# Optimization experiments

Hardware: AMD Instinct MI355X
Metric: run time of the kernel (lower is better)

## Reference

```python
import jax, jax.numpy as jnp
import numpy as np

N_NODES = 100000

def gcn_conv(x, edge_index, W, b):
    # normalize=False GCNConv: out[i] = sum_{(j->i) in E} (x W)[j] + b
    h = x @ W                                   # [N, out_dim]
    src, dst = edge_index[0], edge_index[1]
    msgs = h[src]                               # [E, out_dim]
    agg = jax.ops.segment_sum(msgs, dst, num_segments=N_NODES)
    return agg + b

def setup_inputs() -> dict:
    key = jax.random.key(0)
    k1, k2, k3, k4 = jax.random.split(key, 4)
    x = jax.random.normal(k1, (N_NODES, 512), dtype=jnp.float32)
    edge_index = jax.random.randint(k2, (2, 3200000), 0, N_NODES, dtype=jnp.int64)
    W1 = jax.random.normal(k3, (512, 16), dtype=jnp.float32) * (1.0 / np.sqrt(512))
    b1 = jnp.zeros((16,), dtype=jnp.float32)
    W2 = jax.random.normal(k4, (16, 40), dtype=jnp.float32) * (1.0 / np.sqrt(16))
    b2 = jnp.zeros((40,), dtype=jnp.float32)
    return {"x": x, "edge_index": edge_index, "W1": W1, "b1": b1, "W2": W2, "b2": b2}

def reference(x, edge_index, W1, b1, W2, b2):
    h = jax.nn.relu(gcn_conv(x, edge_index, W1, b1))
    # dropout is identity at inference (training=False)
    out = gcn_conv(h, edge_index, W2, b2)
    return jax.nn.log_softmax(out, axis=1)
```

## Files before the change

kernel.cpp:

```cpp
#include <hip/hip_runtime.h>
#include <math.h>

#define N_NODES 100000
#define N_EDGES 3200000
#define BSHIFT 7
#define BNODES 128
#define NB 782
#define PLACE_BLOCKS 400
#define G1_S 68

typedef float vfloat4 __attribute__((ext_vector_type(4)));

__global__ __launch_bounds__(64) void gemm1_kernel(
    const float* __restrict__ x, const float* __restrict__ W1,
    float* __restrict__ h, int nrows)
{
    __shared__ __align__(16) float xs[32 * G1_S];
    const int t = threadIdx.x;
    const int rbase = blockIdx.x * 64;

    const int kl4  = (t & 7) * 4;
    const int rstg = t >> 3;
    const int swz  = (t & 7) << 3;

    const int rq = t >> 2;
    const int cg = t & 3;
    const float4* __restrict__ w4 = (const float4*)W1;

    float4 acc0 = make_float4(0.f, 0.f, 0.f, 0.f);
    float4 acc1 = acc0, acc2 = acc0, acc3 = acc0;

    vfloat4 pre[8];
    #pragma unroll
    for (int i = 0; i < 8; ++i) {
        int rg = rbase + rstg + i * 8;
        pre[i] = (rg < nrows)
            ? __builtin_nontemporal_load(
                  (const vfloat4*)(x + (size_t)rg * 512 + kl4))
            : (vfloat4){0.f, 0.f, 0.f, 0.f};
    }

    for (int kc = 0; kc < 512; kc += 32) {
        #pragma unroll
        for (int i = 0; i < 8; ++i) {
            int row = (rstg + i * 8) ^ swz;
            float* p = xs + kl4 * G1_S + row;
            p[0 * G1_S] = pre[i].x;
            p[1 * G1_S] = pre[i].y;
            p[2 * G1_S] = pre[i].z;
            p[3 * G1_S] = pre[i].w;
        }
        if (kc + 32 < 512) {
            #pragma unroll
            for (int i = 0; i < 8; ++i) {
                int rg = rbase + rstg + i * 8;
                pre[i] = (rg < nrows)
                    ? __builtin_nontemporal_load(
                          (const vfloat4*)(x + (size_t)rg * 512 + kc + 32 + kl4))
                    : (vfloat4){0.f, 0.f, 0.f, 0.f};
            }
        }

        #pragma unroll
        for (int k4 = 0; k4 < 8; ++k4) {
            const int k0 = k4 * 4;
            const int rr = (rq * 4) ^ (k4 << 3);
            float4 xv0 = *(const float4*)(xs + (k0 + 0) * G1_S + rr);
            float4 xv1 = *(const float4*)(xs + (k0 + 1) * G1_S + rr);
            float4 xv2 = *(const float4*)(xs + (k0 + 2) * G1_S + rr);
            float4 xv3 = *(const float4*)(xs + (k0 + 3) * G1_S + rr);
            float4 wv0 = w4[(kc + k0 + 0) * 4 + cg];
            float4 wv1 = w4[(kc + k0 + 1) * 4 + cg];
            float4 wv2 = w4[(kc + k0 + 2) * 4 + cg];
            float4 wv3 = w4[(kc + k0 + 3) * 4 + cg];

            #define GCN_UPD(xv, wv)                                           \
                acc0.x += (xv).x * (wv).x; acc0.y += (xv).x * (wv).y;         \
                acc0.z += (xv).x * (wv).z; acc0.w += (xv).x * (wv).w;         \
                acc1.x += (xv).y * (wv).x; acc1.y += (xv).y * (wv).y;         \
                acc1.z += (xv).y * (wv).z; acc1.w += (xv).y * (wv).w;         \
                acc2.x += (xv).z * (wv).x; acc2.y += (xv).z * (wv).y;         \
                acc2.z += (xv).z * (wv).z; acc2.w += (xv).z * (wv).w;         \
                acc3.x += (xv).w * (wv).x; acc3.y += (xv).w * (wv).y;         \
                acc3.z += (xv).w * (wv).z; acc3.w += (xv).w * (wv).w;
            GCN_UPD(xv0, wv0)
            GCN_UPD(xv1, wv1)
            GCN_UPD(xv2, wv2)
            GCN_UPD(xv3, wv3)
            #undef GCN_UPD
        }
    }

    {
        int rg = rbase + rq * 4;
        if (rg + 0 < nrows) *(float4*)(h + (size_t)(rg + 0) * 16 + cg * 4) = acc0;
        if (rg + 1 < nrows) *(float4*)(h + (size_t)(rg + 1) * 16 + cg * 4) = acc1;
        if (rg + 2 < nrows) *(float4*)(h + (size_t)(rg + 2) * 16 + cg * 4) = acc2;
        if (rg + 3 < nrows) *(float4*)(h + (size_t)(rg + 3) * 16 + cg * 4) = acc3;
    }
}

__global__ __launch_bounds__(256) void bin_count_kernel(
    const int* __restrict__ ei, int* __restrict__ bucket_cnt)
{
    __shared__ int hist[NB];
    const int t = threadIdx.x;
    for (int i = t; i < NB; i += 256) hist[i] = 0;
    __syncthreads();
    const int stride = gridDim.x * 256;
    for (int e = blockIdx.x * 256 + t; e < N_EDGES; e += stride)
        atomicAdd(&hist[ei[N_EDGES + e] >> BSHIFT], 1);
    __syncthreads();
    for (int i = t; i < NB; i += 256)
        if (hist[i]) atomicAdd(&bucket_cnt[i], hist[i]);
}

__global__ __launch_bounds__(1024) void bucket_scan_kernel(
    const int* __restrict__ bucket_cnt, int* __restrict__ bucket_base,
    int* __restrict__ bucket_cursor)
{
    __shared__ int s[1024];
    const int t = threadIdx.x;
    s[t] = (t < NB) ? bucket_cnt[t] : 0;
    __syncthreads();
    for (int off = 1; off < 1024; off <<= 1) {
        int v = (t >= off) ? s[t - off] : 0;
        __syncthreads();
        s[t] += v;
        __syncthreads();
    }
    if (t < NB) {
        int excl = (t == 0) ? 0 : s[t - 1];
        bucket_base[t]   = excl;
        bucket_cursor[t] = excl;
        if (t == NB - 1) bucket_base[NB] = s[t];
    }
}

__global__ __launch_bounds__(256) void bin_place_kernel(
    const int* __restrict__ ei, int* __restrict__ bucket_cursor,
    int* __restrict__ packed)
{
    __shared__ int cnt[NB];
    __shared__ int base_off[NB];
    __shared__ int cur[NB];
    const int t = threadIdx.x;
    const int chunk = (N_EDGES + PLACE_BLOCKS - 1) / PLACE_BLOCKS;
    const int cs = blockIdx.x * chunk;
    const int ce = min(cs + chunk, N_EDGES);

    for (int i = t; i < NB; i += 256) { cnt[i] = 0; cur[i] = 0; }
    __syncthreads();
    for (int e = cs + t; e < ce; e += 256)
        atomicAdd(&cnt[ei[N_EDGES + e] >> BSHIFT], 1);
    __syncthreads();
    for (int i = t; i < NB; i += 256)
        base_off[i] = cnt[i] ? atomicAdd(&bucket_cursor[i], cnt[i]) : 0;
    __syncthreads();
    for (int e = cs + t; e < ce; e += 256) {
        int s = ei[e];
        int d = ei[N_EDGES + e];
        int b = d >> BSHIFT;
        int pos = base_off[b] + atomicAdd(&cur[b], 1);
        packed[pos] = s | ((d & (BNODES - 1)) << 17);
    }
}

__global__ __launch_bounds__(256) void csr_sort_kernel(
    const int* __restrict__ bucket_base, const int* __restrict__ packed,
    int* __restrict__ csr_src, int* __restrict__ row_ptr)
{
    __shared__ int hist[BNODES];
    __shared__ int excl[BNODES];
    __shared__ int cur[BNODES];
    __shared__ int scan[BNODES];
    const int t = threadIdx.x;
    const int b = blockIdx.x;
    if (t < BNODES) { hist[t] = 0; cur[t] = 0; }
    __syncthreads();

    const int bs = bucket_base[b];
    const int be = bucket_base[b + 1];
    for (int e = bs + t; e < be; e += 256)
        atomicAdd(&hist[packed[e] >> 17], 1);
    __syncthreads();

    if (t < BNODES) scan[t] = hist[t];
    __syncthreads();
    for (int off = 1; off < BNODES; off <<= 1) {
        int v = (t < BNODES && t >= off) ? scan[t - off] : 0;
        __syncthreads();
        if (t < BNODES) scan[t] += v;
        __syncthreads();
    }
    if (t < BNODES) {
        int ex = (t == 0) ? 0 : scan[t - 1];
        excl[t] = ex;
        int g = b * BNODES + t;
        if (g < N_NODES) row_ptr[g] = bs + ex;
    }
    if (b == NB - 1 && t == 0) row_ptr[N_NODES] = N_EDGES;
    __syncthreads();

    for (int e = bs + t; e < be; e += 256) {
        int p  = packed[e];
        int dl = p >> 17;
        int pos = bs + excl[dl] + atomicAdd(&cur[dl], 1);
        csr_src[pos] = p & 0x1FFFF;
    }
}

__global__ __launch_bounds__(256) void gather1_kernel(
    const int* __restrict__ row_ptr, const int* __restrict__ csr_src,
    const float* __restrict__ h, const float* __restrict__ b1,
    float* __restrict__ h1)
{
    const int node = (blockIdx.x * 256 + threadIdx.x) >> 6;
    if (node >= N_NODES) return;
    const int lane = threadIdx.x & 63;
    const int c = lane & 15, slot = lane >> 4;
    const int start = row_ptr[node], end = row_ptr[node + 1];

    float acc = 0.f;
    int e = start;
    for (; e + 16 <= end; e += 16) {
        int s0 = csr_src[e + slot * 4 + 0];
        int s1 = csr_src[e + slot * 4 + 1];
        int s2 = csr_src[e + slot * 4 + 2];
        int s3 = csr_src[e + slot * 4 + 3];
        float v0 = h[s0 * 16 + c];
        float v1 = h[s1 * 16 + c];
        float v2 = h[s2 * 16 + c];
        float v3 = h[s3 * 16 + c];
        acc += (v0 + v1) + (v2 + v3);
    }
    for (; e + 4 <= end; e += 4)
        acc += h[csr_src[e + slot] * 16 + c];
    if (e + slot < end)
        acc += h[csr_src[e + slot] * 16 + c];

    acc += __shfl_xor(acc, 16);
    acc += __shfl_xor(acc, 32);
    if (lane < 16)
        h1[(size_t)node * 16 + c] = fmaxf(acc + b1[c], 0.f);
}

__global__ __launch_bounds__(256) void gather2_kernel(
    const int* __restrict__ row_ptr, const int* __restrict__ csr_src,
    const float* __restrict__ h1, const float* __restrict__ W2,
    const float* __restrict__ b2, float* __restrict__ out)
{
    const int node = (blockIdx.x * 256 + threadIdx.x) >> 6;
    if (node >= N_NODES) return;
    const int lane = threadIdx.x & 63;
    const int c = lane & 15, slot = lane >> 4;

    float w2c[16];
    float b2v = 0.f;
    if (lane < 40) {
        b2v = b2[lane];
        #pragma unroll
        for (int k = 0; k < 16; ++k) w2c[k] = W2[k * 40 + lane];
    } else {
        #pragma unroll
        for (int k = 0; k < 16; ++k) w2c[k] = 0.f;
    }

    const int start = row_ptr[node], end = row_ptr[node + 1];
    float acc = 0.f;
    int e = start;
    for (; e + 16 <= end; e += 16) {
        int s0 = csr_src[e + slot * 4 + 0];
        int s1 = csr_src[e + slot * 4 + 1];
        int s2 = csr_src[e + slot * 4 + 2];
        int s3 = csr_src[e + slot * 4 + 3];
        float v0 = h1[s0 * 16 + c];
        float v1 = h1[s1 * 16 + c];
        float v2 = h1[s2 * 16 + c];
        float v3 = h1[s3 * 16 + c];
        acc += (v0 + v1) + (v2 + v3);
    }
    for (; e + 4 <= end; e += 4)
        acc += h1[csr_src[e + slot] * 16 + c];
    if (e + slot < end)
        acc += h1[csr_src[e + slot] * 16 + c];

    acc += __shfl_xor(acc, 16);
    acc += __shfl_xor(acc, 32);

    float z = b2v;
    #pragma unroll
    for (int k = 0; k < 16; ++k)
        z += __shfl(acc, k) * w2c[k];

    float zm = (lane < 40) ? z : -1e30f;
    #pragma unroll
    for (int off = 1; off < 64; off <<= 1)
        zm = fmaxf(zm, __shfl_xor(zm, off));
    float ex = (lane < 40) ? __expf(z - zm) : 0.f;
    float sum = ex;
    #pragma unroll
    for (int off = 1; off < 64; off <<= 1)
        sum += __shfl_xor(sum, off);
    const float lse = zm + __logf(sum);

    if (lane < 40)
        out[(size_t)node * 40 + lane] = z - lse;
}

extern "C" void kernel_launch(void* const* d_in, const int* in_sizes, int n_in,
                              void* d_out, int out_size, void* d_ws, size_t ws_size,
                              hipStream_t stream)
{
    const float* x  = (const float*)d_in[0];
    const int*   ei = (const int*)d_in[1];
    const float* W1 = (const float*)d_in[2];
    const float* b1 = (const float*)d_in[3];
    const float* W2 = (const float*)d_in[4];
    const float* b2 = (const float*)d_in[5];
    float* out = (float*)d_out;

    float* h      = (float*)d_ws;
    int*   csr    = (int*)(h + (size_t)N_NODES * 16);
    int*   packed = csr + N_EDGES;
    float* h1     = (float*)packed;
    int*   rowp   = packed + N_EDGES;
    int*   bcnt   = rowp + (N_NODES + 1);
    int*   bbase  = bcnt + NB;
    int*   bcur   = bbase + (NB + 1);

    const int gemm1_blocks  = (N_NODES + 63) / 64;
    const int gather_blocks = (N_NODES + 3) / 4;

    hipMemsetAsync(bcnt, 0, NB * sizeof(int), stream);
    bin_count_kernel  <<<256, 256, 0, stream>>>(ei, bcnt);
    bucket_scan_kernel<<<1, 1024, 0, stream>>>(bcnt, bbase, bcur);
    bin_place_kernel  <<<PLACE_BLOCKS, 256, 0, stream>>>(ei, bcur, packed);
    csr_sort_kernel   <<<NB, 256, 0, stream>>>(bbase, packed, csr, rowp);

    gemm1_kernel<<<gemm1_blocks, 64, 0, stream>>>(x, W1, h, N_NODES);

    gather1_kernel<<<gather_blocks, 256, 0, stream>>>(rowp, csr, h, b1, h1);
    gather2_kernel<<<gather_blocks, 256, 0, stream>>>(rowp, csr, h1, W2, b2, out);
}
```

Before: 545.3 us.

## Split first GEMM into tiles co-scheduled with CSR-build kernels

```diff
diff --git a/kernel.cpp b/kernel.cpp
--- a/kernel.cpp
+++ b/kernel.cpp
@@ -8,23 +8,27 @@
 #define NB 782
 #define PLACE_BLOCKS 400
 #define G1_S 68
+#define G1_TILES 1563
+#define TILES_A 280
+#define TILES_B 600
+#define TILES_C (G1_TILES - TILES_A - TILES_B)
+#define BINCNT_BLOCKS 256
 
 typedef float vfloat4 __attribute__((ext_vector_type(4)));
 
-__global__ __launch_bounds__(64) void gemm1_kernel(
+__device__ __forceinline__ void gemm1_tile(
+    int tile, int lane,
     const float* __restrict__ x, const float* __restrict__ W1,
-    float* __restrict__ h, int nrows)
-{
-    __shared__ __align__(16) float xs[32 * G1_S];
-    const int t = threadIdx.x;
-    const int rbase = blockIdx.x * 64;
-
-    const int kl4  = (t & 7) * 4;
-    const int rstg = t >> 3;
-    const int swz  = (t & 7) << 3;
-
-    const int rq = t >> 2;
-    const int cg = t & 3;
+    float* __restrict__ h, float* __restrict__ xs )
+{
+    if (tile >= G1_TILES) return;
+    const int rbase = tile * 64;
+
+    const int kl4  = (lane & 7) * 4;
+    const int rstg = lane >> 3;
+    const int swz  = (lane & 7) << 3;
+    const int rq   = lane >> 2;
+    const int cg   = lane & 3;
     const float4* __restrict__ w4 = (const float4*)W1;
 
     float4 acc0 = make_float4(0.f, 0.f, 0.f, 0.f);
@@ -34,7 +38,7 @@
     #pragma unroll
     for (int i = 0; i < 8; ++i) {
         int rg = rbase + rstg + i * 8;
-        pre[i] = (rg < nrows)
+        pre[i] = (rg < N_NODES)
             ? __builtin_nontemporal_load(
                   (const vfloat4*)(x + (size_t)rg * 512 + kl4))
             : (vfloat4){0.f, 0.f, 0.f, 0.f};
@@ -54,7 +58,7 @@
             #pragma unroll
             for (int i = 0; i < 8; ++i) {
                 int rg = rbase + rstg + i * 8;
-                pre[i] = (rg < nrows)
+                pre[i] = (rg < N_NODES)
                     ? __builtin_nontemporal_load(
                           (const vfloat4*)(x + (size_t)rg * 512 + kc + 32 + kl4))
                     : (vfloat4){0.f, 0.f, 0.f, 0.f};
@@ -93,26 +97,41 @@
 
     {
         int rg = rbase + rq * 4;
-        if (rg + 0 < nrows) *(float4*)(h + (size_t)(rg + 0) * 16 + cg * 4) = acc0;
-        if (rg + 1 < nrows) *(float4*)(h + (size_t)(rg + 1) * 16 + cg * 4) = acc1;
-        if (rg + 2 < nrows) *(float4*)(h + (size_t)(rg + 2) * 16 + cg * 4) = acc2;
-        if (rg + 3 < nrows) *(float4*)(h + (size_t)(rg + 3) * 16 + cg * 4) = acc3;
-    }
-}
-
-__global__ __launch_bounds__(256) void bin_count_kernel(
+        if (rg + 0 < N_NODES) *(float4*)(h + (size_t)(rg + 0) * 16 + cg * 4) = acc0;
+        if (rg + 1 < N_NODES) *(float4*)(h + (size_t)(rg + 1) * 16 + cg * 4) = acc1;
+        if (rg + 2 < N_NODES) *(float4*)(h + (size_t)(rg + 2) * 16 + cg * 4) = acc2;
+        if (rg + 3 < N_NODES) *(float4*)(h + (size_t)(rg + 3) * 16 + cg * 4) = acc3;
+    }
+}
+
+union ShA {
+    float xs[4][32 * G1_S];
+    int hist[NB];
+};
+
+__global__ __launch_bounds__(256) void stageA_kernel(
+    const float* __restrict__ x, const float* __restrict__ W1,
+    float* __restrict__ h,
     const int* __restrict__ ei, int* __restrict__ bucket_cnt)
 {
-    __shared__ int hist[NB];
+    __shared__ __align__(16) ShA sh;
     const int t = threadIdx.x;
-    for (int i = t; i < NB; i += 256) hist[i] = 0;
-    __syncthreads();
-    const int stride = gridDim.x * 256;
-    for (int e = blockIdx.x * 256 + t; e < N_EDGES; e += stride)
-        atomicAdd(&hist[ei[N_EDGES + e] >> BSHIFT], 1);
-    __syncthreads();
-    for (int i = t; i < NB; i += 256)
-        if (hist[i]) atomicAdd(&bucket_cnt[i], hist[i]);
+
+    if (blockIdx.x < BINCNT_BLOCKS) {
+        for (int i = t; i < NB; i += 256) sh.hist[i] = 0;
+        __syncthreads();
+        const int stride = BINCNT_BLOCKS * 256;
+        for (int e = blockIdx.x * 256 + t; e < N_EDGES; e += stride)
+            atomicAdd(&sh.hist[ei[N_EDGES + e] >> BSHIFT], 1);
+        __syncthreads();
+        for (int i = t; i < NB; i += 256)
+            if (sh.hist[i]) atomicAdd(&bucket_cnt[i], sh.hist[i]);
+    } else {
+        const int w = t >> 6;
+        const int tile = (blockIdx.x - BINCNT_BLOCKS) * 4 + w;
+        if (tile < TILES_A)
+            gemm1_tile(tile, t & 63, x, W1, h, sh.xs[w]);
+    }
 }
 
 __global__ __launch_bounds__(1024) void bucket_scan_kernel(
@@ -137,76 +156,101 @@
     }
 }
 
-__global__ __launch_bounds__(256) void bin_place_kernel(
+union ShB {
+    float xs[4][32 * G1_S];
+    struct { int cnt[NB]; int base_off[NB]; int cur[NB]; } p;
+};
+
+__global__ __launch_bounds__(256) void stageB_kernel(
+    const float* __restrict__ x, const float* __restrict__ W1,
+    float* __restrict__ h,
     const int* __restrict__ ei, int* __restrict__ bucket_cursor,
     int* __restrict__ packed)
 {
-    __shared__ int cnt[NB];
-    __shared__ int base_off[NB];
-    __shared__ int cur[NB];
+    __shared__ __align__(16) ShB sh;
     const int t = threadIdx.x;
-    const int chunk = (N_EDGES + PLACE_BLOCKS - 1) / PLACE_BLOCKS;
-    const int cs = blockIdx.x * chunk;
-    const int ce = min(cs + chunk, N_EDGES);
-
-    for (int i = t; i < NB; i += 256) { cnt[i] = 0; cur[i] = 0; }
-    __syncthreads();
-    for (int e = cs + t; e < ce; e += 256)
-        atomicAdd(&cnt[ei[N_EDGES + e] >> BSHIFT], 1);
-    __syncthreads();
-    for (int i = t; i < NB; i += 256)
-        base_off[i] = cnt[i] ? atomicAdd(&bucket_cursor[i], cnt[i]) : 0;
-    __syncthreads();
-    for (int e = cs + t; e < ce; e += 256) {
-        int s = ei[e];
-        int d = ei[N_EDGES + e];
-        int b = d >> BSHIFT;
-        int pos = base_off[b] + atomicAdd(&cur[b], 1);
-        packed[pos] = s | ((d & (BNODES - 1)) << 17);
-    }
-}
-
-__global__ __launch_bounds__(256) void csr_sort_kernel(
+
+    if (blockIdx.x < PLACE_BLOCKS) {
+        const int chunk = (N_EDGES + PLACE_BLOCKS - 1) / PLACE_BLOCKS;
+        const int cs = blockIdx.x * chunk;
+        const int ce = min(cs + chunk, N_EDGES);
+
+        for (int i = t; i < NB; i += 256) { sh.p.cnt[i] = 0; sh.p.cur[i] = 0; }
+        __syncthreads();
+        for (int e = cs + t; e < ce; e += 256)
+            atomicAdd(&sh.p.cnt[ei[N_EDGES + e] >> BSHIFT], 1);
+        __syncthreads();
+        for (int i = t; i < NB; i += 256)
+            sh.p.base_off[i] = sh.p.cnt[i] ? atomicAdd(&bucket_cursor[i], sh.p.cnt[i]) : 0;
+        __syncthreads();
+        for (int e = cs + t; e < ce; e += 256) {
+            int s = ei[e];
+            int d = ei[N_EDGES + e];
+            int b = d >> BSHIFT;
+            int pos = sh.p.base_off[b] + atomicAdd(&sh.p.cur[b], 1);
+            packed[pos] = s | ((d & (BNODES - 1)) << 17);
+        }
+    } else {
+        const int w = t >> 6;
+        const int tile = TILES_A + (blockIdx.x - PLACE_BLOCKS) * 4 + w;
+        if (tile < TILES_A + TILES_B)
+            gemm1_tile(tile, t & 63, x, W1, h, sh.xs[w]);
+    }
+}
+
+union ShC {
+    float xs[4][32 * G1_S];
+    struct { int hist[BNODES]; int excl[BNODES]; int cur[BNODES]; int scan[BNODES]; } c;
+};
+
+__global__ __launch_bounds__(256) void stageC_kernel(
+    const float* __restrict__ x, const float* __restrict__ W1,
+    float* __restrict__ h,
     const int* __restrict__ bucket_base, const int* __restrict__ packed,
     int* __restrict__ csr_src, int* __restrict__ row_ptr)
 {
-    __shared__ int hist[BNODES];
-    __shared__ int excl[BNODES];
-    __shared__ int cur[BNODES];
-    __shared__ int scan[BNODES];
+    __shared__ __align__(16) ShC sh;
     const int t = threadIdx.x;
     const int b = blockIdx.x;
-    if (t < BNODES) { hist[t] = 0; cur[t] = 0; }
-    __syncthreads();
-
-    const int bs = bucket_base[b];
-    const int be = bucket_base[b + 1];
-    for (int e = bs + t; e < be; e += 256)
-        atomicAdd(&hist[packed[e] >> 17], 1);
-    __syncthreads();
-
-    if (t < BNODES) scan[t] = hist[t];
-    __syncthreads();
-    for (int off = 1; off < BNODES; off <<= 1) {
-        int v = (t < BNODES && t >= off) ? scan[t - off] : 0;
-        __syncthreads();
-        if (t < BNODES) scan[t] += v;
-        __syncthreads();
-    }
-    if (t < BNODES) {
-        int ex = (t == 0) ? 0 : scan[t - 1];
-        excl[t] = ex;
-        int g = b * BNODES + t;
-        if (g < N_NODES) row_ptr[g] = bs + ex;
-    }
-    if (b == NB - 1 && t == 0) row_ptr[N_NODES] = N_EDGES;
-    __syncthreads();
-
-    for (int e = bs + t; e < be; e += 256) {
-        int p  = packed[e];
-        int dl = p >> 17;
-        int pos = bs + excl[dl] + atomicAdd(&cur[dl], 1);
-        csr_src[pos] = p & 0x1FFFF;
+
+    if (b < NB) {
+        if (t < BNODES) { sh.c.hist[t] = 0; sh.c.cur[t] = 0; }
+        __syncthreads();
+
+        const int bs = bucket_base[b];
+        const int be = bucket_base[b + 1];
+        for (int e = bs + t; e < be; e += 256)
+            atomicAdd(&sh.c.hist[packed[e] >> 17], 1);
+        __syncthreads();
+
+        if (t < BNODES) sh.c.scan[t] = sh.c.hist[t];
+        __syncthreads();
+        for (int off = 1; off < BNODES; off <<= 1) {
+            int v = (t < BNODES && t >= off) ? sh.c.scan[t - off] : 0;
+            __syncthreads();
+            if (t < BNODES) sh.c.scan[t] += v;
+            __syncthreads();
+        }
+        if (t < BNODES) {
+            int ex = (t == 0) ? 0 : sh.c.scan[t - 1];
+            sh.c.excl[t] = ex;
+            int g = b * BNODES + t;
+            if (g < N_NODES) row_ptr[g] = bs + ex;
+        }
+        if (b == NB - 1 && t == 0) row_ptr[N_NODES] = N_EDGES;
+        __syncthreads();
+
+        for (int e = bs + t; e < be; e += 256) {
+            int p  = packed[e];
+            int dl = p >> 17;
+            int pos = bs + sh.c.excl[dl] + atomicAdd(&sh.c.cur[dl], 1);
+            csr_src[pos] = p & 0x1FFFF;
+        }
+    } else {
+        const int w = t >> 6;
+        const int tile = TILES_A + TILES_B + (b - NB) * 4 + w;
+        if (tile < G1_TILES)
+            gemm1_tile(tile, t & 63, x, W1, h, sh.xs[w]);
     }
 }
 
@@ -329,16 +373,16 @@
     int*   bbase  = bcnt + NB;
     int*   bcur   = bbase + (NB + 1);
 
-    const int gemm1_blocks  = (N_NODES + 63) / 64;
+    const int stageA_blocks = BINCNT_BLOCKS + (TILES_A + 3) / 4;
+    const int stageB_blocks = PLACE_BLOCKS + (TILES_B + 3) / 4;
+    const int stageC_blocks = NB + (TILES_C + 3) / 4;
     const int gather_blocks = (N_NODES + 3) / 4;
 
     hipMemsetAsync(bcnt, 0, NB * sizeof(int), stream);
-    bin_count_kernel  <<<256, 256, 0, stream>>>(ei, bcnt);
+    stageA_kernel     <<<stageA_blocks, 256, 0, stream>>>(x, W1, h, ei, bcnt);
     bucket_scan_kernel<<<1, 1024, 0, stream>>>(bcnt, bbase, bcur);
-    bin_place_kernel  <<<PLACE_BLOCKS, 256, 0, stream>>>(ei, bcur, packed);
-    csr_sort_kernel   <<<NB, 256, 0, stream>>>(bbase, packed, csr, rowp);
-
-    gemm1_kernel<<<gemm1_blocks, 64, 0, stream>>>(x, W1, h, N_NODES);
+    stageB_kernel     <<<stageB_blocks, 256, 0, stream>>>(x, W1, h, ei, bcur, packed);
+    stageC_kernel     <<<stageC_blocks, 256, 0, stream>>>(x, W1, h, bbase, packed, csr, rowp);
 
     gather1_kernel<<<gather_blocks, 256, 0, stream>>>(rowp, csr, h, b1, h1);
     gather2_kernel<<<gather_blocks, 256, 0, stream>>>(rowp, csr, h1, W2, b2, out);
```

After: 595.7 us. +9.2%, slower.

## Drop per-node CSR sort; aggregate bucketed edges via LDS atomics per block

Applied to the files above, without the earlier changes.

```diff
diff --git a/kernel.cpp b/kernel.cpp
--- a/kernel.cpp
+++ b/kernel.cpp
@@ -8,6 +8,7 @@
 #define NB 782
 #define PLACE_BLOCKS 400
 #define G1_S 68
+#define AGG_S 17
 
 typedef float vfloat4 __attribute__((ext_vector_type(4)));
 
@@ -22,9 +23,8 @@
     const int kl4  = (t & 7) * 4;
     const int rstg = t >> 3;
     const int swz  = (t & 7) << 3;
-
-    const int rq = t >> 2;
-    const int cg = t & 3;
+    const int rq   = t >> 2;
+    const int cg   = t & 3;
     const float4* __restrict__ w4 = (const float4*)W1;
 
     float4 acc0 = make_float4(0.f, 0.f, 0.f, 0.f);
@@ -166,94 +166,69 @@
     }
 }
 
-__global__ __launch_bounds__(256) void csr_sort_kernel(
+__global__ __launch_bounds__(256) void gatherA_kernel(
     const int* __restrict__ bucket_base, const int* __restrict__ packed,
-    int* __restrict__ csr_src, int* __restrict__ row_ptr)
-{
-    __shared__ int hist[BNODES];
-    __shared__ int excl[BNODES];
-    __shared__ int cur[BNODES];
-    __shared__ int scan[BNODES];
-    const int t = threadIdx.x;
-    const int b = blockIdx.x;
-    if (t < BNODES) { hist[t] = 0; cur[t] = 0; }
-    __syncthreads();
-
-    const int bs = bucket_base[b];
-    const int be = bucket_base[b + 1];
-    for (int e = bs + t; e < be; e += 256)
-        atomicAdd(&hist[packed[e] >> 17], 1);
-    __syncthreads();
-
-    if (t < BNODES) scan[t] = hist[t];
-    __syncthreads();
-    for (int off = 1; off < BNODES; off <<= 1) {
-        int v = (t < BNODES && t >= off) ? scan[t - off] : 0;
-        __syncthreads();
-        if (t < BNODES) scan[t] += v;
-        __syncthreads();
-    }
-    if (t < BNODES) {
-        int ex = (t == 0) ? 0 : scan[t - 1];
-        excl[t] = ex;
-        int g = b * BNODES + t;
-        if (g < N_NODES) row_ptr[g] = bs + ex;
-    }
-    if (b == NB - 1 && t == 0) row_ptr[N_NODES] = N_EDGES;
-    __syncthreads();
-
-    for (int e = bs + t; e < be; e += 256) {
-        int p  = packed[e];
-        int dl = p >> 17;
-        int pos = bs + excl[dl] + atomicAdd(&cur[dl], 1);
-        csr_src[pos] = p & 0x1FFFF;
-    }
-}
-
-__global__ __launch_bounds__(256) void gather1_kernel(
-    const int* __restrict__ row_ptr, const int* __restrict__ csr_src,
     const float* __restrict__ h, const float* __restrict__ b1,
     float* __restrict__ h1)
 {
-    const int node = (blockIdx.x * 256 + threadIdx.x) >> 6;
-    if (node >= N_NODES) return;
-    const int lane = threadIdx.x & 63;
-    const int c = lane & 15, slot = lane >> 4;
-    const int start = row_ptr[node], end = row_ptr[node + 1];
-
-    float acc = 0.f;
-    int e = start;
-    for (; e + 16 <= end; e += 16) {
-        int s0 = csr_src[e + slot * 4 + 0];
-        int s1 = csr_src[e + slot * 4 + 1];
-        int s2 = csr_src[e + slot * 4 + 2];
-        int s3 = csr_src[e + slot * 4 + 3];
-        float v0 = h[s0 * 16 + c];
-        float v1 = h[s1 * 16 + c];
-        float v2 = h[s2 * 16 + c];
-        float v3 = h[s3 * 16 + c];
-        acc += (v0 + v1) + (v2 + v3);
-    }
-    for (; e + 4 <= end; e += 4)
-        acc += h[csr_src[e + slot] * 16 + c];
-    if (e + slot < end)
-        acc += h[csr_src[e + slot] * 16 + c];
-
-    acc += __shfl_xor(acc, 16);
-    acc += __shfl_xor(acc, 32);
-    if (lane < 16)
-        h1[(size_t)node * 16 + c] = fmaxf(acc + b1[c], 0.f);
-}
-
-__global__ __launch_bounds__(256) void gather2_kernel(
-    const int* __restrict__ row_ptr, const int* __restrict__ csr_src,
+    __shared__ float agg[BNODES * AGG_S];
+    const int t = threadIdx.x;
+    const int b = blockIdx.x;
+    const int c = t & 15, slot = t >> 4;
+
+    #pragma unroll
+    for (int i = 0; i < 9; ++i) {
+        int idx = i * 256 + t;
+        if (idx < BNODES * AGG_S) agg[idx] = 0.f;
+    }
+    __syncthreads();
+
+    const int bs = bucket_base[b];
+    const int nE = bucket_base[b + 1] - bs;
+
+    int i = slot;
+    for (; i + 48 < nE; i += 64) {
+        int p0 = packed[bs + i];
+        int p1 = packed[bs + i + 16];
+        int p2 = packed[bs + i + 32];
+        int p3 = packed[bs + i + 48];
+        float v0 = h[(p0 & 0x1FFFF) * 16 + c];
+        float v1 = h[(p1 & 0x1FFFF) * 16 + c];
+        float v2 = h[(p2 & 0x1FFFF) * 16 + c];
+        float v3 = h[(p3 & 0x1FFFF) * 16 + c];
+        atomicAdd(&agg[(p0 >> 17) * AGG_S + c], v0);
+        atomicAdd(&agg[(p1 >> 17) * AGG_S + c], v1);
+        atomicAdd(&agg[(p2 >> 17) * AGG_S + c], v2);
+        atomicAdd(&agg[(p3 >> 17) * AGG_S + c], v3);
+    }
+    for (; i < nE; i += 16) {
+        int p = packed[bs + i];
+        float v = h[(p & 0x1FFFF) * 16 + c];
+        atomicAdd(&agg[(p >> 17) * AGG_S + c], v);
+    }
+    __syncthreads();
+
+    #pragma unroll
+    for (int j = 0; j < 8; ++j) {
+        int idx = j * 256 + t;
+        int dl = idx >> 4, cc = idx & 15;
+        int node = b * BNODES + dl;
+        if (node < N_NODES)
+            h1[(size_t)node * 16 + cc] =
+                fmaxf(agg[dl * AGG_S + cc] + b1[cc], 0.f);
+    }
+}
+
+__global__ __launch_bounds__(256) void gatherB_kernel(
+    const int* __restrict__ bucket_base, const int* __restrict__ packed,
     const float* __restrict__ h1, const float* __restrict__ W2,
     const float* __restrict__ b2, float* __restrict__ out)
 {
-    const int node = (blockIdx.x * 256 + threadIdx.x) >> 6;
-    if (node >= N_NODES) return;
-    const int lane = threadIdx.x & 63;
-    const int c = lane & 15, slot = lane >> 4;
+    __shared__ float agg[BNODES * AGG_S];
+    const int t = threadIdx.x;
+    const int b = blockIdx.x;
+    const int c = t & 15, slot = t >> 4;
+    const int lane = t & 63, w = t >> 6;
 
     float w2c[16];
     float b2v = 0.f;
@@ -266,46 +241,62 @@
         for (int k = 0; k < 16; ++k) w2c[k] = 0.f;
     }
 
-    const int start = row_ptr[node], end = row_ptr[node + 1];
-    float acc = 0.f;
-    int e = start;
-    for (; e + 16 <= end; e += 16) {
-        int s0 = csr_src[e + slot * 4 + 0];
-        int s1 = csr_src[e + slot * 4 + 1];
-        int s2 = csr_src[e + slot * 4 + 2];
-        int s3 = csr_src[e + slot * 4 + 3];
-        float v0 = h1[s0 * 16 + c];
-        float v1 = h1[s1 * 16 + c];
-        float v2 = h1[s2 * 16 + c];
-        float v3 = h1[s3 * 16 + c];
-        acc += (v0 + v1) + (v2 + v3);
-    }
-    for (; e + 4 <= end; e += 4)
-        acc += h1[csr_src[e + slot] * 16 + c];
-    if (e + slot < end)
-        acc += h1[csr_src[e + slot] * 16 + c];
-
-    acc += __shfl_xor(acc, 16);
-    acc += __shfl_xor(acc, 32);
-
-    float z = b2v;
     #pragma unroll
-    for (int k = 0; k < 16; ++k)
-        z += __shfl(acc, k) * w2c[k];
-
-    float zm = (lane < 40) ? z : -1e30f;
-    #pragma unroll
-    for (int off = 1; off < 64; off <<= 1)
-        zm = fmaxf(zm, __shfl_xor(zm, off));
-    float ex = (lane < 40) ? __expf(z - zm) : 0.f;
-    float sum = ex;
-    #pragma unroll
-    for (int off = 1; off < 64; off <<= 1)
-        sum += __shfl_xor(sum, off);
-    const float lse = zm + __logf(sum);
-
-    if (lane < 40)
-        out[(size_t)node * 40 + lane] = z - lse;
+    for (int i = 0; i < 9; ++i) {
+        int idx = i * 256 + t;
+        if (idx < BNODES * AGG_S) agg[idx] = 0.f;
+    }
+    __syncthreads();
+
+    const int bs = bucket_base[b];
+    const int nE = bucket_base[b + 1] - bs;
+
+    int i = slot;
+    for (; i + 48 < nE; i += 64) {
+        int p0 = packed[bs + i];
+        int p1 = packed[bs + i + 16];
+        int p2 = packed[bs + i + 32];
+        int p3 = packed[bs + i + 48];
+        float v0 = h1[(p0 & 0x1FFFF) * 16 + c];
+        float v1 = h1[(p1 & 0x1FFFF) * 16 + c];
+        float v2 = h1[(p2 & 0x1FFFF) * 16 + c];
+        float v3 = h1[(p3 & 0x1FFFF) * 16 + c];
+        atomicAdd(&agg[(p0 >> 17) * AGG_S + c], v0);
+        atomicAdd(&agg[(p1 >> 17) * AGG_S + c], v1);
+        atomicAdd(&agg[(p2 >> 17) * AGG_S + c], v2);
+        atomicAdd(&agg[(p3 >> 17) * AGG_S + c], v3);
+    }
+    for (; i < nE; i += 16) {
+        int p = packed[bs + i];
+        float v = h1[(p & 0x1FFFF) * 16 + c];
+        atomicAdd(&agg[(p >> 17) * AGG_S + c], v);
+    }
+    __syncthreads();
+
+    for (int q = 0; q < 32; ++q) {
+        const int dl = w * 32 + q;
+        const int node = b * BNODES + dl;
+        if (node >= N_NODES) break;
+
+        float z = b2v;
+        #pragma unroll
+        for (int k = 0; k < 16; ++k)
+            z += agg[dl * AGG_S + k] * w2c[k];
+
+        float zm = (lane < 40) ? z : -1e30f;
+        #pragma unroll
+        for (int off = 1; off < 64; off <<= 1)
+            zm = fmaxf(zm, __shfl_xor(zm, off));
+        float ex = (lane < 40) ? __expf(z - zm) : 0.f;
+        float sum = ex;
+        #pragma unroll
+        for (int off = 1; off < 64; off <<= 1)
+            sum += __shfl_xor(sum, off);
+        const float lse = zm + __logf(sum);
+
+        if (lane < 40)
+            out[(size_t)node * 40 + lane] = z - lse;
+    }
 }
 
 extern "C" void kernel_launch(void* const* d_in, const int* in_sizes, int n_in,
@@ -321,25 +312,21 @@
     float* out = (float*)d_out;
 
     float* h      = (float*)d_ws;
-    int*   csr    = (int*)(h + (size_t)N_NODES * 16);
-    int*   packed = csr + N_EDGES;
-    float* h1     = (float*)packed;
-    int*   rowp   = packed + N_EDGES;
-    int*   bcnt   = rowp + (N_NODES + 1);
+    int*   packed = (int*)(h + (size_t)N_NODES * 16);
+    float* h1     = (float*)(packed + N_EDGES);
+    int*   bcnt   = (int*)(h1 + (size_t)N_NODES * 16);
     int*   bbase  = bcnt + NB;
     int*   bcur   = bbase + (NB + 1);
 
-    const int gemm1_blocks  = (N_NODES + 63) / 64;
-    const int gather_blocks = (N_NODES + 3) / 4;
+    const int gemm1_blocks = (N_NODES + 63) / 64;
 
     hipMemsetAsync(bcnt, 0, NB * sizeof(int), stream);
     bin_count_kernel  <<<256, 256, 0, stream>>>(ei, bcnt);
     bucket_scan_kernel<<<1, 1024, 0, stream>>>(bcnt, bbase, bcur);
     bin_place_kernel  <<<PLACE_BLOCKS, 256, 0, stream>>>(ei, bcur, packed);
-    csr_sort_kernel   <<<NB, 256, 0, stream>>>(bbase, packed, csr, rowp);
 
     gemm1_kernel<<<gemm1_blocks, 64, 0, stream>>>(x, W1, h, N_NODES);
 
-    gather1_kernel<<<gather_blocks, 256, 0, stream>>>(rowp, csr, h, b1, h1);
-    gather2_kernel<<<gather_blocks, 256, 0, stream>>>(rowp, csr, h1, W2, b2, out);
-}
+    gatherA_kernel<<<NB, 256, 0, stream>>>(bbase, packed, h, b1, h1);
+    gatherB_kernel<<<NB, 256, 0, stream>>>(bbase, packed, h1, W2, b2, out);
+}
```

After: 1.107 ms. 103% more time.

## Replace bucket count/scan passes with fixed-capacity per-bucket edge slots

Applied to the files above, without the earlier changes.

```diff
diff --git a/kernel.cpp b/kernel.cpp
--- a/kernel.cpp
+++ b/kernel.cpp
@@ -8,6 +8,7 @@
 #define NB 782
 #define PLACE_BLOCKS 400
 #define G1_S 68
+#define CAP 8192
 
 typedef float vfloat4 __attribute__((ext_vector_type(4)));
 
@@ -22,9 +23,8 @@
     const int kl4  = (t & 7) * 4;
     const int rstg = t >> 3;
     const int swz  = (t & 7) << 3;
-
-    const int rq = t >> 2;
-    const int cg = t & 3;
+    const int rq   = t >> 2;
+    const int cg   = t & 3;
     const float4* __restrict__ w4 = (const float4*)W1;
 
     float4 acc0 = make_float4(0.f, 0.f, 0.f, 0.f);
@@ -100,45 +100,8 @@
     }
 }
 
-__global__ __launch_bounds__(256) void bin_count_kernel(
-    const int* __restrict__ ei, int* __restrict__ bucket_cnt)
-{
-    __shared__ int hist[NB];
-    const int t = threadIdx.x;
-    for (int i = t; i < NB; i += 256) hist[i] = 0;
-    __syncthreads();
-    const int stride = gridDim.x * 256;
-    for (int e = blockIdx.x * 256 + t; e < N_EDGES; e += stride)
-        atomicAdd(&hist[ei[N_EDGES + e] >> BSHIFT], 1);
-    __syncthreads();
-    for (int i = t; i < NB; i += 256)
-        if (hist[i]) atomicAdd(&bucket_cnt[i], hist[i]);
-}
-
-__global__ __launch_bounds__(1024) void bucket_scan_kernel(
-    const int* __restrict__ bucket_cnt, int* __restrict__ bucket_base,
-    int* __restrict__ bucket_cursor)
-{
-    __shared__ int s[1024];
-    const int t = threadIdx.x;
-    s[t] = (t < NB) ? bucket_cnt[t] : 0;
-    __syncthreads();
-    for (int off = 1; off < 1024; off <<= 1) {
-        int v = (t >= off) ? s[t - off] : 0;
-        __syncthreads();
-        s[t] += v;
-        __syncthreads();
-    }
-    if (t < NB) {
-        int excl = (t == 0) ? 0 : s[t - 1];
-        bucket_base[t]   = excl;
-        bucket_cursor[t] = excl;
-        if (t == NB - 1) bucket_base[NB] = s[t];
-    }
-}
-
-__global__ __launch_bounds__(256) void bin_place_kernel(
-    const int* __restrict__ ei, int* __restrict__ bucket_cursor,
+__global__ __launch_bounds__(256) void place_kernel(
+    const int* __restrict__ ei, int* __restrict__ gcur,
     int* __restrict__ packed)
 {
     __shared__ int cnt[NB];
@@ -155,20 +118,21 @@
         atomicAdd(&cnt[ei[N_EDGES + e] >> BSHIFT], 1);
     __syncthreads();
     for (int i = t; i < NB; i += 256)
-        base_off[i] = cnt[i] ? atomicAdd(&bucket_cursor[i], cnt[i]) : 0;
+        base_off[i] = cnt[i] ? atomicAdd(&gcur[i], cnt[i]) : 0;
     __syncthreads();
     for (int e = cs + t; e < ce; e += 256) {
         int s = ei[e];
         int d = ei[N_EDGES + e];
         int b = d >> BSHIFT;
         int pos = base_off[b] + atomicAdd(&cur[b], 1);
-        packed[pos] = s | ((d & (BNODES - 1)) << 17);
+        if (pos < CAP)
+            packed[(size_t)b * CAP + pos] = s | ((d & (BNODES - 1)) << 17);
     }
 }
 
 __global__ __launch_bounds__(256) void csr_sort_kernel(
-    const int* __restrict__ bucket_base, const int* __restrict__ packed,
-    int* __restrict__ csr_src, int* __restrict__ row_ptr)
+    const int* __restrict__ gcur, const int* __restrict__ packed,
+    int* __restrict__ csr_src, int* __restrict__ rowp)
 {
     __shared__ int hist[BNODES];
     __shared__ int excl[BNODES];
@@ -179,10 +143,10 @@
     if (t < BNODES) { hist[t] = 0; cur[t] = 0; }
     __syncthreads();
 
-    const int bs = bucket_base[b];
-    const int be = bucket_base[b + 1];
-    for (int e = bs + t; e < be; e += 256)
-        atomicAdd(&hist[packed[e] >> 17], 1);
+    const int bs = b * CAP;
+    const int cntb = min(gcur[b], CAP);
+    for (int e = t; e < cntb; e += 256)
+        atomicAdd(&hist[packed[bs + e] >> 17], 1);
     __syncthreads();
 
     if (t < BNODES) scan[t] = hist[t];
@@ -196,14 +160,13 @@
     if (t < BNODES) {
         int ex = (t == 0) ? 0 : scan[t - 1];
         excl[t] = ex;
-        int g = b * BNODES + t;
-        if (g < N_NODES) row_ptr[g] = bs + ex;
-    }
-    if (b == NB - 1 && t == 0) row_ptr[N_NODES] = N_EDGES;
-    __syncthreads();
-
-    for (int e = bs + t; e < be; e += 256) {
-        int p  = packed[e];
+        rowp[b * 129 + t] = bs + ex;
+        if (t == 0) rowp[b * 129 + 128] = bs + cntb;
+    }
+    __syncthreads();
+
+    for (int e = t; e < cntb; e += 256) {
+        int p  = packed[bs + e];
         int dl = p >> 17;
         int pos = bs + excl[dl] + atomicAdd(&cur[dl], 1);
         csr_src[pos] = p & 0x1FFFF;
@@ -211,7 +174,7 @@
 }
 
 __global__ __launch_bounds__(256) void gather1_kernel(
-    const int* __restrict__ row_ptr, const int* __restrict__ csr_src,
+    const int* __restrict__ rowp, const int* __restrict__ csr_src,
     const float* __restrict__ h, const float* __restrict__ b1,
     float* __restrict__ h1)
 {
@@ -219,7 +182,8 @@
     if (node >= N_NODES) return;
     const int lane = threadIdx.x & 63;
     const int c = lane & 15, slot = lane >> 4;
-    const int start = row_ptr[node], end = row_ptr[node + 1];
+    const int rp = (node >> BSHIFT) * 129 + (node & (BNODES - 1));
+    const int start = rowp[rp], end = rowp[rp + 1];
 
     float acc = 0.f;
     int e = start;
@@ -246,7 +210,7 @@
 }
 
 __global__ __launch_bounds__(256) void gather2_kernel(
-    const int* __restrict__ row_ptr, const int* __restrict__ csr_src,
+    const int* __restrict__ rowp, const int* __restrict__ csr_src,
     const float* __restrict__ h1, const float* __restrict__ W2,
     const float* __restrict__ b2, float* __restrict__ out)
 {
@@ -266,7 +230,8 @@
         for (int k = 0; k < 16; ++k) w2c[k] = 0.f;
     }
 
-    const int start = row_ptr[node], end = row_ptr[node + 1];
+    const int rp = (node >> BSHIFT) * 129 + (node & (BNODES - 1));
+    const int start = rowp[rp], end = rowp[rp + 1];
     float acc = 0.f;
     int e = start;
     for (; e + 16 <= end; e += 16) {
@@ -321,22 +286,18 @@
     float* out = (float*)d_out;
 
     float* h      = (float*)d_ws;
-    int*   csr    = (int*)(h + (size_t)N_NODES * 16);
-    int*   packed = csr + N_EDGES;
+    int*   packed = (int*)(h + (size_t)N_NODES * 16);
+    int*   csr    = packed + (size_t)NB * CAP;
+    int*   rowp   = csr + (size_t)NB * CAP;
+    int*   gcur   = rowp + NB * 129 + 1;
     float* h1     = (float*)packed;
-    int*   rowp   = packed + N_EDGES;
-    int*   bcnt   = rowp + (N_NODES + 1);
-    int*   bbase  = bcnt + NB;
-    int*   bcur   = bbase + (NB + 1);
 
     const int gemm1_blocks  = (N_NODES + 63) / 64;
     const int gather_blocks = (N_NODES + 3) / 4;
 
-    hipMemsetAsync(bcnt, 0, NB * sizeof(int), stream);
-    bin_count_kernel  <<<256, 256, 0, stream>>>(ei, bcnt);
-    bucket_scan_kernel<<<1, 1024, 0, stream>>>(bcnt, bbase, bcur);
-    bin_place_kernel  <<<PLACE_BLOCKS, 256, 0, stream>>>(ei, bcur, packed);
-    csr_sort_kernel   <<<NB, 256, 0, stream>>>(bbase, packed, csr, rowp);
+    hipMemsetAsync(gcur, 0, NB * sizeof(int), stream);
+    place_kernel   <<<PLACE_BLOCKS, 256, 0, stream>>>(ei, gcur, packed);
+    csr_sort_kernel<<<NB, 256, 0, stream>>>(gcur, packed, csr, rowp);
 
     gemm1_kernel<<<gemm1_blocks, 64, 0, stream>>>(x, W1, h, N_NODES);
 
```

After: 525.5 us. -3.6%, faster.
